# Optimization experiments

Hardware: AMD Instinct MI355X
Metric: run time of the kernel (lower is better)

Reference implementation:

```python
import jax, jax.numpy as jnp
import numpy as np

# Inner-product factors for Cl(1,3) (Minkowski metric diag(+,-,-,-)).
# For blade e_b, <~e_b e_b>_0 = product of the metric signs of its constituent vectors.
# Blade order: [1, e0,e1,e2,e3, e01,e02,e03,e12,e13,e23, e012,e013,e023,e123, e0123]
_IPF = jnp.array([1, 1, -1, -1, -1, -1, -1, -1, 1, 1, 1, 1, 1, 1, -1, -1], dtype=jnp.float32)

B, H, N, CMV, CS = 4, 8, 2048, 8, 16


def setup_inputs() -> dict:
    key = jax.random.key(0)
    ks = jax.random.split(key, 6)
    f = lambda k, s: jax.random.normal(k, s, dtype=jnp.float32)
    return {
        "q_mv": f(ks[0], (B, H, N, CMV, 16)),
        "k_mv": f(ks[1], (B, H, N, CMV, 16)),
        "v_mv": f(ks[2], (B, H, N, CMV, 16)),
        "q_s": f(ks[3], (B, H, N, CS)),
        "k_s": f(ks[4], (B, H, N, CS)),
        "v_s": f(ks[5], (B, H, N, CS)),
    }


def reference(q_mv, k_mv, v_mv, q_s, k_s, v_s):
    b, h, n, cmv, _ = q_mv.shape
    cs = q_s.shape[-1]
    cmv_out = v_mv.shape[-2]
    cs_out = v_s.shape[-1]
    # GA inner product on mv part = euclidean dot after applying metric factors to queries
    q = jnp.concatenate([(q_mv * _IPF).reshape(b, h, n, cmv * 16), q_s], axis=-1)
    k = jnp.concatenate([k_mv.reshape(b, h, n, cmv * 16), k_s], axis=-1)
    v = jnp.concatenate([v_mv.reshape(b, h, n, cmv_out * 16), v_s], axis=-1)
    scale = 1.0 / np.sqrt(q.shape[-1]).astype(np.float32)  # torch SDPA default scale
    scores = jnp.einsum("bhid,bhjd->bhij", q, k) * scale  # [B,H,N,N]
    attn = jax.nn.softmax(scores, axis=-1)
    out = jnp.einsum("bhij,bhjd->bhid", attn, v)
    out_mv = out[..., : cmv_out * 16].reshape(b, h, n, cmv_out, 16)
    out_s = out[..., cmv_out * 16 : cmv_out * 16 + cs_out]
    return out_mv, out_s
```

## Files before the change

kernel.cpp:

```cpp
#include <hip/hip_runtime.h>
#include <cstdint>
#include <math.h>


#define BH    32
#define N_    2048
#define DMV   128
#define DS    16
#define D_    144
#define BM    128
#define BN    64
#define NKIT  (N_ / BN)
#define KSTR  168
#define VSTR  72
#define PSTR  72
#define KP_BYTES  ((size_t)BH * N_ * KSTR * 2)
#define QSCALE 0.12022458674074693f

typedef __bf16 bf16_8 __attribute__((ext_vector_type(8)));
typedef __bf16 bf16_4 __attribute__((ext_vector_type(4)));
typedef __bf16 bf16_2 __attribute__((ext_vector_type(2)));
typedef float  f32x4  __attribute__((ext_vector_type(4)));

#define GLOAD_LDS16(g, l)                                                     \
  __builtin_amdgcn_global_load_lds(                                           \
      (const __attribute__((address_space(1))) void*)(g),                     \
      (__attribute__((address_space(3))) void*)(l), 16, 0, 0)

__device__ __forceinline__ f32x4 mfma16(bf16_8 a, bf16_8 b, f32x4 c) {
  return __builtin_amdgcn_mfma_f32_16x16x32_bf16(a, b, c, 0, 0, 0);
}

__device__ __forceinline__ bf16_4 cvt4(f32x4 x) {
  bf16_4 w; w[0]=(__bf16)x[0]; w[1]=(__bf16)x[1]; w[2]=(__bf16)x[2]; w[3]=(__bf16)x[3];
  return w;
}

__global__ __launch_bounds__(256)
void pack_k(const float* __restrict__ kmv, const float* __restrict__ ks_,
            __bf16* __restrict__ kp) {
  const unsigned g = blockIdx.x * 256 + threadIdx.x;
  const unsigned row = g / 21u, seg = g - row * 21u;
  bf16_8 o;
  if (seg < 16) {
    const f32x4* p = (const f32x4*)(kmv + (size_t)row * DMV + seg * 8);
    f32x4 a = p[0], b = p[1];
#pragma unroll
    for (int j = 0; j < 8; ++j) o[j] = (__bf16)((j < 4) ? a[j] : b[j - 4]);
  } else if (seg < 18) {
    const f32x4* p = (const f32x4*)(ks_ + (size_t)row * DS + (seg - 16) * 8);
    f32x4 a = p[0], b = p[1];
#pragma unroll
    for (int j = 0; j < 8; ++j) o[j] = (__bf16)((j < 4) ? a[j] : b[j - 4]);
  } else {
#pragma unroll
    for (int j = 0; j < 8; ++j) o[j] = (__bf16)0.0f;
  }
  *(bf16_8*)(kp + (size_t)row * KSTR + seg * 8) = o;
}

#define TSTR 156
__global__ __launch_bounds__(256)
void pack_vt(const float* __restrict__ vmv, const float* __restrict__ vs,
             __bf16* __restrict__ vt) {
  __shared__ __bf16 sT[64 * TSTR];
  const int tile = blockIdx.x;
  const int t = threadIdx.x;
  const int n = t >> 2, c = t & 3;
  const float* mv = vmv + (size_t)(tile * 64 + n) * DMV;
  const float* s  = vs  + (size_t)(tile * 64 + n) * DS;
  __bf16* row = &sT[n * TSTR];
  if (c < 3) {
#pragma unroll
    for (int i = 0; i < 9; ++i)
      *(bf16_4*)&row[c * 36 + 4 * i] = cvt4(*(const f32x4*)(mv + c * 36 + 4 * i));
  } else {
#pragma unroll
    for (int i = 0; i < 5; ++i)
      *(bf16_4*)&row[108 + 4 * i] = cvt4(*(const f32x4*)(mv + 108 + 4 * i));
#pragma unroll
    for (int i = 0; i < 4; ++i)
      *(bf16_4*)&row[128 + 4 * i] = cvt4(*(const f32x4*)(s + 4 * i));
  }
  __syncthreads();
  __bf16* vtt = vt + (size_t)tile * (D_ * VSTR);
#pragma unroll
  for (int k = 0; k < 18; ++k) {
    int idx = t + 256 * k;
    int d = idx >> 5, j = idx & 31;
    bf16_2 p; p[0] = sT[(2 * j) * TSTR + d]; p[1] = sT[(2 * j + 1) * TSTR + d];
    *(bf16_2*)&vtt[d * VSTR + 2 * j] = p;
  }
}

__device__ __forceinline__ bf16_8 load_q_frag(const float* qmv_row, const float* qs_row, int k0) {
  bf16_8 f;
  if (k0 < DMV) {
    const f32x4* p = (const f32x4*)(qmv_row + k0);
    f32x4 a = p[0], b = p[1];
    int hi = k0 & 8;
#pragma unroll
    for (int j = 0; j < 8; ++j) {
      float v = (j < 4) ? a[j] : b[j - 4];
      bool pos = hi ? (j < 6) : (j < 2);
      f[j] = (__bf16)(v * (pos ? QSCALE : -QSCALE));
    }
  } else if (k0 < D_) {
    const f32x4* p = (const f32x4*)(qs_row + (k0 - DMV));
    f32x4 a = p[0], b = p[1];
#pragma unroll
    for (int j = 0; j < 8; ++j) {
      float v = (j < 4) ? a[j] : b[j - 4];
      f[j] = (__bf16)(v * QSCALE);
    }
  } else {
#pragma unroll
    for (int j = 0; j < 8; ++j) f[j] = (__bf16)0.0f;
  }
  return f;
}

__global__ __launch_bounds__(512, 4)
void geo_attn_kernel(const float* __restrict__ q_mv, const float* __restrict__ q_s,
                     const __bf16* __restrict__ kp, const __bf16* __restrict__ vt,
                     float* __restrict__ out)
{
  __shared__ __bf16 sK[BN * KSTR];
  __shared__ __bf16 sVT[D_ * VSTR];

  const int tid  = threadIdx.x;
  const int w    = tid >> 6;
  const int lane = tid & 63;
  const int l15  = lane & 15;
  const int quad = lane >> 4;
  const int bh    = blockIdx.y;
  const int qbase = blockIdx.x * BM;
  const size_t bh_n = (size_t)bh * N_;

  __bf16* sP = sK + w * (16 * PSTR);

  bf16_8 qf[5];
  {
    int mrow = qbase + 16 * w + l15;
    const float* qmv_row = q_mv + (bh_n + mrow) * DMV;
    const float* qs_row  = q_s  + (bh_n + mrow) * DS;
#pragma unroll
    for (int ks = 0; ks < 5; ++ks)
      qf[ks] = load_q_frag(qmv_row, qs_row, ks * 32 + quad * 8);
  }

  f32x4 of[9];
#pragma unroll
  for (int n9 = 0; n9 < 9; ++n9)
#pragma unroll
    for (int r = 0; r < 4; ++r) of[n9][r] = 0.0f;
  float m_i = -INFINITY, l_i = 0.0f;

  const __bf16* kbase = kp + bh_n * KSTR;

  for (int it = 0; it < NKIT; ++it) {
    {
      const __bf16* kt  = kbase + (size_t)(it * BN) * KSTR;
      const __bf16* vtt = vt + (size_t)(bh * NKIT + it) * (D_ * VSTR);
      for (int i = w; i < 21; i += 8)
        GLOAD_LDS16(kt + i * 512 + lane * 8, &sK[i * 512 + lane * 8]);
      for (int i = w; i < 20; i += 8)
        GLOAD_LDS16(vtt + i * 512 + lane * 8, &sVT[i * 512 + lane * 8]);
      if (w == 0 && lane < 16)
        GLOAD_LDS16(vtt + 20 * 512 + lane * 8, &sVT[20 * 512 + lane * 8]);
    }
    __syncthreads();

    f32x4 sf[4];
#pragma unroll
    for (int nt = 0; nt < 4; ++nt)
#pragma unroll
      for (int r = 0; r < 4; ++r) sf[nt][r] = 0.0f;
#pragma unroll
    for (int ks = 0; ks < 5; ++ks) {
#pragma unroll
      for (int nt = 0; nt < 4; ++nt) {
        bf16_8 kb = *(const bf16_8*)&sK[(nt * 16 + l15) * KSTR + ks * 32 + quad * 8];
        sf[nt] = mfma16(kb, qf[ks], sf[nt]);
      }
    }
    __syncthreads();

    {
      float mx = sf[0][0];
#pragma unroll
      for (int nt = 0; nt < 4; ++nt)
#pragma unroll
        for (int r = 0; r < 4; ++r) mx = fmaxf(mx, sf[nt][r]);
      mx = fmaxf(mx, __shfl_xor(mx, 16));
      mx = fmaxf(mx, __shfl_xor(mx, 32));
      float mnew = fmaxf(m_i, mx);
      float al = __builtin_amdgcn_exp2f(m_i - mnew);
      m_i = mnew;
      float rs = 0.0f;
#pragma unroll
      for (int nt = 0; nt < 4; ++nt)
#pragma unroll
        for (int r = 0; r < 4; ++r) {
          float p = __builtin_amdgcn_exp2f(sf[nt][r] - mnew);
          sf[nt][r] = p;
          rs += p;
        }
      rs += __shfl_xor(rs, 16);
      rs += __shfl_xor(rs, 32);
      l_i = l_i * al + rs;

#pragma unroll
      for (int nt = 0; nt < 4; ++nt) {
        bf16_4 pw;
#pragma unroll
        for (int r = 0; r < 4; ++r) pw[r] = (__bf16)sf[nt][r];
        *(bf16_4*)&sP[l15 * PSTR + nt * 16 + quad * 4] = pw;
      }
      asm volatile("s_waitcnt lgkmcnt(0)" ::: "memory");

      float alr[4];
#pragma unroll
      for (int r = 0; r < 4; ++r) alr[r] = __shfl(al, 20 * quad + r);
#pragma unroll
      for (int n9 = 0; n9 < 9; ++n9)
#pragma unroll
        for (int r = 0; r < 4; ++r) of[n9][r] *= alr[r];
    }

#pragma unroll
    for (int ks = 0; ks < 2; ++ks) {
      bf16_8 pa = *(const bf16_8*)&sP[l15 * PSTR + ks * 32 + quad * 8];
#pragma unroll
      for (int n9 = 0; n9 < 9; ++n9) {
        bf16_8 vb = *(const bf16_8*)&sVT[(n9 * 16 + l15) * VSTR + ks * 32 + quad * 8];
        of[n9] = mfma16(pa, vb, of[n9]);
      }
    }
    __syncthreads();
  }

  float* out_mv = out;
  float* out_s  = out + (size_t)BH * N_ * DMV;
  float linv[4];
#pragma unroll
  for (int r = 0; r < 4; ++r)
    linv[r] = __builtin_amdgcn_rcpf(__shfl(l_i, 20 * quad + r));
#pragma unroll
  for (int n9 = 0; n9 < 9; ++n9) {
#pragma unroll
    for (int r = 0; r < 4; ++r) {
      int row = qbase + 16 * w + quad * 4 + r;
      float val = of[n9][r] * linv[r];
      if (n9 < 8) out_mv[(bh_n + row) * DMV + n9 * 16 + l15] = val;
      else        out_s [(bh_n + row) * DS + l15] = val;
    }
  }
}

extern "C" void kernel_launch(void* const* d_in, const int* in_sizes, int n_in,
                              void* d_out, int out_size, void* d_ws, size_t ws_size,
                              hipStream_t stream) {
  (void)in_sizes; (void)n_in; (void)out_size; (void)ws_size;
  const float* q_mv = (const float*)d_in[0];
  const float* k_mv = (const float*)d_in[1];
  const float* v_mv = (const float*)d_in[2];
  const float* q_s  = (const float*)d_in[3];
  const float* k_s  = (const float*)d_in[4];
  const float* v_s  = (const float*)d_in[5];
  float* out = (float*)d_out;

  __bf16* kp = (__bf16*)d_ws;
  __bf16* vt = (__bf16*)((char*)d_ws + KP_BYTES);

  pack_k<<<(BH * N_ * 21) / 256, 256, 0, stream>>>(k_mv, k_s, kp);
  pack_vt<<<BH * NKIT, 256, 0, stream>>>(v_mv, v_s, vt);

  dim3 grid(N_ / BM, BH);
  geo_attn_kernel<<<grid, 512, 0, stream>>>(q_mv, q_s, kp, vt, out);
}
```

Measured before the change: 271.0 us.

## Switch attention to 32x32x16 MFMA with register-resident P and lazy rescaling

The attention kernel moves from 16x16x32 to 32x32x16 bf16 MFMA tiles with 4 waves of 32 query rows each. The P matrix is passed between the two matmuls in registers via cvt_pk and permlane32_swap instead of a round trip through LDS, which also removes one barrier per iteration. It adds a lazy max update that skips rescaling the accumulator while the new max stays within a threshold, and raises MFMA issue priority with setprio. The two pack kernels are merged into one launch, the K padding stride is narrowed, and the V transpose is done directly in LDS. Risks include lower occupancy from the larger accumulators and fewer waves per block, and possible bf16 overflow in the lazily scaled exponentials.

```diff
diff --git a/kernel.cpp b/kernel.cpp
--- a/kernel.cpp
+++ b/kernel.cpp
@@ -11,85 +11,90 @@
 #define BM    128
 #define BN    64
 #define NKIT  (N_ / BN)
-#define KSTR  168
+#define KSTR  152
 #define VSTR  72
-#define PSTR  72
-#define KP_BYTES  ((size_t)BH * N_ * KSTR * 2)
+#define SVROWS 160
+#define KCHUNKS (BN * KSTR / 8)
+#define VCHUNKS (D_ * VSTR / 8)
+#define KP_BYTES ((size_t)BH * N_ * KSTR * 2)
 #define QSCALE 0.12022458674074693f
+#define KPACK_BLOCKS (BH * N_ * 19 / 256)
 
 typedef __bf16 bf16_8 __attribute__((ext_vector_type(8)));
-typedef __bf16 bf16_4 __attribute__((ext_vector_type(4)));
-typedef __bf16 bf16_2 __attribute__((ext_vector_type(2)));
 typedef float  f32x4  __attribute__((ext_vector_type(4)));
+typedef float  f32x16 __attribute__((ext_vector_type(16)));
 
 #define GLOAD_LDS16(g, l)                                                     \
   __builtin_amdgcn_global_load_lds(                                           \
       (const __attribute__((address_space(1))) void*)(g),                     \
       (__attribute__((address_space(3))) void*)(l), 16, 0, 0)
 
-__device__ __forceinline__ f32x4 mfma16(bf16_8 a, bf16_8 b, f32x4 c) {
-  return __builtin_amdgcn_mfma_f32_16x16x32_bf16(a, b, c, 0, 0, 0);
-}
-
-__device__ __forceinline__ bf16_4 cvt4(f32x4 x) {
-  bf16_4 w; w[0]=(__bf16)x[0]; w[1]=(__bf16)x[1]; w[2]=(__bf16)x[2]; w[3]=(__bf16)x[3];
-  return w;
+__device__ __forceinline__ f32x16 mfma32(bf16_8 a, bf16_8 b, f32x16 c) {
+  return __builtin_amdgcn_mfma_f32_32x32x16_bf16(a, b, c, 0, 0, 0);
 }
 
 __global__ __launch_bounds__(256)
-void pack_k(const float* __restrict__ kmv, const float* __restrict__ ks_,
-            __bf16* __restrict__ kp) {
-  const unsigned g = blockIdx.x * 256 + threadIdx.x;
-  const unsigned row = g / 21u, seg = g - row * 21u;
-  bf16_8 o;
-  if (seg < 16) {
-    const f32x4* p = (const f32x4*)(kmv + (size_t)row * DMV + seg * 8);
-    f32x4 a = p[0], b = p[1];
-#pragma unroll
-    for (int j = 0; j < 8; ++j) o[j] = (__bf16)((j < 4) ? a[j] : b[j - 4]);
-  } else if (seg < 18) {
-    const f32x4* p = (const f32x4*)(ks_ + (size_t)row * DS + (seg - 16) * 8);
-    f32x4 a = p[0], b = p[1];
-#pragma unroll
-    for (int j = 0; j < 8; ++j) o[j] = (__bf16)((j < 4) ? a[j] : b[j - 4]);
-  } else {
-#pragma unroll
-    for (int j = 0; j < 8; ++j) o[j] = (__bf16)0.0f;
-  }
-  *(bf16_8*)(kp + (size_t)row * KSTR + seg * 8) = o;
-}
-
-#define TSTR 156
-__global__ __launch_bounds__(256)
-void pack_vt(const float* __restrict__ vmv, const float* __restrict__ vs,
-             __bf16* __restrict__ vt) {
-  __shared__ __bf16 sT[64 * TSTR];
-  const int tile = blockIdx.x;
+void pack_kv(const float* __restrict__ kmv, const float* __restrict__ ks_,
+             const float* __restrict__ vmv, const float* __restrict__ vs,
+             __bf16* __restrict__ kp, __bf16* __restrict__ vt) {
+  __shared__ __align__(16) __bf16 sT[D_ * VSTR];
   const int t = threadIdx.x;
+  const int b = blockIdx.x;
+  if (b < KPACK_BLOCKS) {
+    const unsigned g = b * 256u + t;
+    const unsigned row = g / 19u, seg = g - row * 19u;
+    bf16_8 o;
+    if (seg < 16) {
+      const f32x4* p = (const f32x4*)(kmv + (size_t)row * DMV + seg * 8);
+      f32x4 a = p[0], bb = p[1];
+#pragma unroll
+      for (int j = 0; j < 8; ++j) o[j] = (__bf16)((j < 4) ? a[j] : bb[j - 4]);
+    } else if (seg < 18) {
+      const f32x4* p = (const f32x4*)(ks_ + (size_t)row * DS + (seg - 16) * 8);
+      f32x4 a = p[0], bb = p[1];
+#pragma unroll
+      for (int j = 0; j < 8; ++j) o[j] = (__bf16)((j < 4) ? a[j] : bb[j - 4]);
+    } else {
+#pragma unroll
+      for (int j = 0; j < 8; ++j) o[j] = (__bf16)0.0f;
+    }
+    *(bf16_8*)(kp + (size_t)row * KSTR + seg * 8) = o;
+    return;
+  }
+  const int tile = b - KPACK_BLOCKS;
   const int n = t >> 2, c = t & 3;
   const float* mv = vmv + (size_t)(tile * 64 + n) * DMV;
-  const float* s  = vs  + (size_t)(tile * 64 + n) * DS;
-  __bf16* row = &sT[n * TSTR];
+  const float* sv = vs  + (size_t)(tile * 64 + n) * DS;
   if (c < 3) {
 #pragma unroll
-    for (int i = 0; i < 9; ++i)
-      *(bf16_4*)&row[c * 36 + 4 * i] = cvt4(*(const f32x4*)(mv + c * 36 + 4 * i));
+    for (int i = 0; i < 9; ++i) {
+      f32x4 q = *(const f32x4*)(mv + c * 36 + 4 * i);
+#pragma unroll
+      for (int j = 0; j < 4; ++j) sT[(c * 36 + 4 * i + j) * VSTR + n] = (__bf16)q[j];
+    }
   } else {
 #pragma unroll
-    for (int i = 0; i < 5; ++i)
-      *(bf16_4*)&row[108 + 4 * i] = cvt4(*(const f32x4*)(mv + 108 + 4 * i));
-#pragma unroll
-    for (int i = 0; i < 4; ++i)
-      *(bf16_4*)&row[128 + 4 * i] = cvt4(*(const f32x4*)(s + 4 * i));
+    for (int i = 0; i < 5; ++i) {
+      f32x4 q = *(const f32x4*)(mv + 108 + 4 * i);
+#pragma unroll
+      for (int j = 0; j < 4; ++j) sT[(108 + 4 * i + j) * VSTR + n] = (__bf16)q[j];
+    }
+#pragma unroll
+    for (int i = 0; i < 4; ++i) {
+      f32x4 q = *(const f32x4*)(sv + 4 * i);
+#pragma unroll
+      for (int j = 0; j < 4; ++j) sT[(DMV + 4 * i + j) * VSTR + n] = (__bf16)q[j];
+    }
   }
   __syncthreads();
   __bf16* vtt = vt + (size_t)tile * (D_ * VSTR);
 #pragma unroll
-  for (int k = 0; k < 18; ++k) {
-    int idx = t + 256 * k;
-    int d = idx >> 5, j = idx & 31;
-    bf16_2 p; p[0] = sT[(2 * j) * TSTR + d]; p[1] = sT[(2 * j + 1) * TSTR + d];
-    *(bf16_2*)&vtt[d * VSTR + 2 * j] = p;
+  for (int s = 0; s < 5; ++s) {
+    int idx = t + 256 * s;
+    if (idx < D_ * 8) {
+      int d = idx >> 3, jc = idx & 7;
+      *(bf16_8*)&vtt[d * VSTR + jc * 8] = *(const bf16_8*)&sT[d * VSTR + jc * 8];
+    }
   }
 }
 
@@ -98,14 +103,14 @@
   if (k0 < DMV) {
     const f32x4* p = (const f32x4*)(qmv_row + k0);
     f32x4 a = p[0], b = p[1];
-    int hi = k0 & 8;
+    int hi8 = k0 & 8;
 #pragma unroll
     for (int j = 0; j < 8; ++j) {
       float v = (j < 4) ? a[j] : b[j - 4];
-      bool pos = hi ? (j < 6) : (j < 2);
+      bool pos = hi8 ? (j < 6) : (j < 2);
       f[j] = (__bf16)(v * (pos ? QSCALE : -QSCALE));
     }
-  } else if (k0 < D_) {
+  } else {
     const f32x4* p = (const f32x4*)(qs_row + (k0 - DMV));
     f32x4 a = p[0], b = p[1];
 #pragma unroll
@@ -113,47 +118,47 @@
       float v = (j < 4) ? a[j] : b[j - 4];
       f[j] = (__bf16)(v * QSCALE);
     }
-  } else {
-#pragma unroll
-    for (int j = 0; j < 8; ++j) f[j] = (__bf16)0.0f;
   }
   return f;
 }
 
-__global__ __launch_bounds__(512, 4)
+__global__ __launch_bounds__(256, 2)
 void geo_attn_kernel(const float* __restrict__ q_mv, const float* __restrict__ q_s,
                      const __bf16* __restrict__ kp, const __bf16* __restrict__ vt,
                      float* __restrict__ out)
 {
-  __shared__ __bf16 sK[BN * KSTR];
-  __shared__ __bf16 sVT[D_ * VSTR];
+  __shared__ __align__(16) __bf16 sK[BN * KSTR];
+  __shared__ __align__(16) __bf16 sVT[SVROWS * VSTR];
 
   const int tid  = threadIdx.x;
   const int w    = tid >> 6;
   const int lane = tid & 63;
-  const int l15  = lane & 15;
-  const int quad = lane >> 4;
+  const int c32  = lane & 31;
+  const int hi   = lane >> 5;
   const int bh    = blockIdx.y;
   const int qbase = blockIdx.x * BM;
   const size_t bh_n = (size_t)bh * N_;
 
-  __bf16* sP = sK + w * (16 * PSTR);
-
-  bf16_8 qf[5];
+  if (tid < 144) {
+    f32x4 z = {0.f, 0.f, 0.f, 0.f};
+    *(f32x4*)((char*)sVT + D_ * VSTR * 2 + tid * 16) = z;
+  }
+
+  bf16_8 qf[9];
   {
-    int mrow = qbase + 16 * w + l15;
+    const int mrow = qbase + w * 32 + c32;
     const float* qmv_row = q_mv + (bh_n + mrow) * DMV;
     const float* qs_row  = q_s  + (bh_n + mrow) * DS;
 #pragma unroll
-    for (int ks = 0; ks < 5; ++ks)
-      qf[ks] = load_q_frag(qmv_row, qs_row, ks * 32 + quad * 8);
-  }
-
-  f32x4 of[9];
-#pragma unroll
-  for (int n9 = 0; n9 < 9; ++n9)
-#pragma unroll
-    for (int r = 0; r < 4; ++r) of[n9][r] = 0.0f;
+    for (int ks = 0; ks < 9; ++ks)
+      qf[ks] = load_q_frag(qmv_row, qs_row, ks * 16 + hi * 8);
+  }
+
+  f32x16 of[5];
+#pragma unroll
+  for (int dt = 0; dt < 5; ++dt)
+#pragma unroll
+    for (int r = 0; r < 16; ++r) of[dt][r] = 0.0f;
   float m_i = -INFINITY, l_i = 0.0f;
 
   const __bf16* kbase = kp + bh_n * KSTR;
@@ -162,99 +167,105 @@
     {
       const __bf16* kt  = kbase + (size_t)(it * BN) * KSTR;
       const __bf16* vtt = vt + (size_t)(bh * NKIT + it) * (D_ * VSTR);
-      for (int i = w; i < 21; i += 8)
-        GLOAD_LDS16(kt + i * 512 + lane * 8, &sK[i * 512 + lane * 8]);
-      for (int i = w; i < 20; i += 8)
-        GLOAD_LDS16(vtt + i * 512 + lane * 8, &sVT[i * 512 + lane * 8]);
-      if (w == 0 && lane < 16)
-        GLOAD_LDS16(vtt + 20 * 512 + lane * 8, &sVT[20 * 512 + lane * 8]);
+#pragma unroll
+      for (int s = 0; s < 4; ++s)
+        GLOAD_LDS16(kt + (tid + 256 * s) * 8, &sK[(tid + 256 * s) * 8]);
+      if (tid < KCHUNKS - 1024)
+        GLOAD_LDS16(kt + (tid + 1024) * 8, &sK[(tid + 1024) * 8]);
+#pragma unroll
+      for (int s = 0; s < 5; ++s)
+        GLOAD_LDS16(vtt + (tid + 256 * s) * 8, &sVT[(tid + 256 * s) * 8]);
+      if (tid < VCHUNKS - 1280)
+        GLOAD_LDS16(vtt + (tid + 1280) * 8, &sVT[(tid + 1280) * 8]);
     }
     __syncthreads();
 
-    f32x4 sf[4];
-#pragma unroll
-    for (int nt = 0; nt < 4; ++nt)
-#pragma unroll
-      for (int r = 0; r < 4; ++r) sf[nt][r] = 0.0f;
-#pragma unroll
-    for (int ks = 0; ks < 5; ++ks) {
-#pragma unroll
-      for (int nt = 0; nt < 4; ++nt) {
-        bf16_8 kb = *(const bf16_8*)&sK[(nt * 16 + l15) * KSTR + ks * 32 + quad * 8];
-        sf[nt] = mfma16(kb, qf[ks], sf[nt]);
-      }
-    }
-    __syncthreads();
-
+    f32x16 sf[2];
+#pragma unroll
+    for (int nt = 0; nt < 2; ++nt)
+#pragma unroll
+      for (int r = 0; r < 16; ++r) sf[nt][r] = 0.0f;
+    __builtin_amdgcn_s_setprio(1);
+#pragma unroll
+    for (int ks = 0; ks < 9; ++ks) {
+      bf16_8 kb0 = *(const bf16_8*)&sK[(c32)      * KSTR + ks * 16 + hi * 8];
+      bf16_8 kb1 = *(const bf16_8*)&sK[(32 + c32) * KSTR + ks * 16 + hi * 8];
+      sf[0] = mfma32(kb0, qf[ks], sf[0]);
+      sf[1] = mfma32(kb1, qf[ks], sf[1]);
+    }
+    __builtin_amdgcn_s_setprio(0);
+
+    float al = 1.0f, m_use;
     {
       float mx = sf[0][0];
 #pragma unroll
-      for (int nt = 0; nt < 4; ++nt)
-#pragma unroll
-        for (int r = 0; r < 4; ++r) mx = fmaxf(mx, sf[nt][r]);
-      mx = fmaxf(mx, __shfl_xor(mx, 16));
+      for (int r = 1; r < 16; ++r) mx = fmaxf(mx, sf[0][r]);
+#pragma unroll
+      for (int r = 0; r < 16; ++r) mx = fmaxf(mx, sf[1][r]);
       mx = fmaxf(mx, __shfl_xor(mx, 32));
-      float mnew = fmaxf(m_i, mx);
-      float al = __builtin_amdgcn_exp2f(m_i - mnew);
-      m_i = mnew;
+
+      if (__all(mx <= m_i + 8.0f)) {
+        m_use = m_i;
+      } else {
+        float mnew = fmaxf(m_i, mx);
+        al = __builtin_amdgcn_exp2f(m_i - mnew);
+        m_i = mnew; m_use = mnew;
+#pragma unroll
+        for (int r = 0; r < 16; ++r) {
+          float a = __shfl(al, (r & 3) + 8 * (r >> 2) + 4 * hi);
+#pragma unroll
+          for (int dt = 0; dt < 5; ++dt) of[dt][r] *= a;
+        }
+      }
       float rs = 0.0f;
 #pragma unroll
-      for (int nt = 0; nt < 4; ++nt)
-#pragma unroll
-        for (int r = 0; r < 4; ++r) {
-          float p = __builtin_amdgcn_exp2f(sf[nt][r] - mnew);
+      for (int nt = 0; nt < 2; ++nt)
+#pragma unroll
+        for (int r = 0; r < 16; ++r) {
+          float p = __builtin_amdgcn_exp2f(sf[nt][r] - m_use);
           sf[nt][r] = p;
           rs += p;
         }
-      rs += __shfl_xor(rs, 16);
       rs += __shfl_xor(rs, 32);
       l_i = l_i * al + rs;
-
-#pragma unroll
-      for (int nt = 0; nt < 4; ++nt) {
-        bf16_4 pw;
-#pragma unroll
-        for (int r = 0; r < 4; ++r) pw[r] = (__bf16)sf[nt][r];
-        *(bf16_4*)&sP[l15 * PSTR + nt * 16 + quad * 4] = pw;
+    }
+
+#pragma unroll
+    for (int ks = 0; ks < 4; ++ks) {
+      const int nt = ks >> 1;
+      const int Ra = 8 * (ks & 1);
+      unsigned x0, x1, y0, y1;
+      asm("v_cvt_pk_bf16_f32 %0, %1, %2" : "=v"(x0) : "v"(sf[nt][Ra + 0]), "v"(sf[nt][Ra + 1]));
+      asm("v_cvt_pk_bf16_f32 %0, %1, %2" : "=v"(x1) : "v"(sf[nt][Ra + 2]), "v"(sf[nt][Ra + 3]));
+      asm("v_cvt_pk_bf16_f32 %0, %1, %2" : "=v"(y0) : "v"(sf[nt][Ra + 4]), "v"(sf[nt][Ra + 5]));
+      asm("v_cvt_pk_bf16_f32 %0, %1, %2" : "=v"(y1) : "v"(sf[nt][Ra + 6]), "v"(sf[nt][Ra + 7]));
+      auto s0 = __builtin_amdgcn_permlane32_swap(x0, y0, false, false);
+      auto s1 = __builtin_amdgcn_permlane32_swap(x1, y1, false, false);
+      union { unsigned u[4]; bf16_8 v; } pu;
+      pu.u[0] = s0[0]; pu.u[1] = s1[0]; pu.u[2] = s0[1]; pu.u[3] = s1[1];
+      __builtin_amdgcn_s_setprio(1);
+#pragma unroll
+      for (int dt = 0; dt < 5; ++dt) {
+        bf16_8 vb = *(const bf16_8*)&sVT[(dt * 32 + c32) * VSTR + ks * 16 + hi * 8];
+        of[dt] = mfma32(pu.v, vb, of[dt]);
       }
-      asm volatile("s_waitcnt lgkmcnt(0)" ::: "memory");
-
-      float alr[4];
-#pragma unroll
-      for (int r = 0; r < 4; ++r) alr[r] = __shfl(al, 20 * quad + r);
-#pragma unroll
-      for (int n9 = 0; n9 < 9; ++n9)
-#pragma unroll
-        for (int r = 0; r < 4; ++r) of[n9][r] *= alr[r];
-    }
-
-#pragma unroll
-    for (int ks = 0; ks < 2; ++ks) {
-      bf16_8 pa = *(const bf16_8*)&sP[l15 * PSTR + ks * 32 + quad * 8];
-#pragma unroll
-      for (int n9 = 0; n9 < 9; ++n9) {
-        bf16_8 vb = *(const bf16_8*)&sVT[(n9 * 16 + l15) * VSTR + ks * 32 + quad * 8];
-        of[n9] = mfma16(pa, vb, of[n9]);
-      }
+      __builtin_amdgcn_s_setprio(0);
     }
     __syncthreads();
   }
 
   float* out_mv = out;
   float* out_s  = out + (size_t)BH * N_ * DMV;
-  float linv[4];
-#pragma unroll
-  for (int r = 0; r < 4; ++r)
-    linv[r] = __builtin_amdgcn_rcpf(__shfl(l_i, 20 * quad + r));
-#pragma unroll
-  for (int n9 = 0; n9 < 9; ++n9) {
-#pragma unroll
-    for (int r = 0; r < 4; ++r) {
-      int row = qbase + 16 * w + quad * 4 + r;
-      float val = of[n9][r] * linv[r];
-      if (n9 < 8) out_mv[(bh_n + row) * DMV + n9 * 16 + l15] = val;
-      else        out_s [(bh_n + row) * DS + l15] = val;
-    }
+#pragma unroll
+  for (int r = 0; r < 16; ++r) {
+    const int ml  = (r & 3) + 8 * (r >> 2) + 4 * hi;
+    const float linv = __builtin_amdgcn_rcpf(__shfl(l_i, ml));
+    const int row = qbase + w * 32 + ml;
+#pragma unroll
+    for (int dt = 0; dt < 4; ++dt)
+      out_mv[(bh_n + row) * DMV + dt * 32 + c32] = of[dt][r] * linv;
+    if (c32 < DS)
+      out_s[(bh_n + row) * DS + c32] = of[4][r] * linv;
   }
 }
 
@@ -273,9 +284,8 @@
   __bf16* kp = (__bf16*)d_ws;
   __bf16* vt = (__bf16*)((char*)d_ws + KP_BYTES);
 
-  pack_k<<<(BH * N_ * 21) / 256, 256, 0, stream>>>(k_mv, k_s, kp);
-  pack_vt<<<BH * NKIT, 256, 0, stream>>>(v_mv, v_s, vt);
+  pack_kv<<<KPACK_BLOCKS + BH * NKIT, 256, 0, stream>>>(k_mv, k_s, v_mv, v_s, kp, vt);
 
   dim3 grid(N_ / BM, BH);
-  geo_attn_kernel<<<grid, 512, 0, stream>>>(q_mv, q_s, kp, vt, out);
-}
+  geo_attn_kernel<<<grid, 256, 0, stream>>>(q_mv, q_s, kp, vt, out);
+}
```

Result: faster. 244.0 us (-9.9%).
